# Performance work log

Measured on AMD Instinct MI355X. Metric: run time of the kernel, lower is better.

## Reference

```python
import jax, jax.numpy as jnp
import numpy as np

N_NODES = 200000
N_EDGES = 500000
D = 128          # n_feature = lig_dim = prot_dim
HID = 512        # n_mdn_hidden
N_LAYERS = 3     # n_mdn_layers
G = 10           # n_mdn_gauss
BN_EPS = 1e-5


def setup_inputs() -> dict:
    key = jax.random.key(0)
    ks = jax.random.split(key, 20)
    inp = {
        "h": jax.random.normal(ks[0], (N_NODES, D), dtype=jnp.float32),
        "pl_edge": jax.random.randint(ks[1], (2, N_EDGES), 0, N_NODES),
        "pl_dist": jax.random.uniform(ks[2], (N_EDGES,), dtype=jnp.float32) * 10.0,
        # MLP params
        "W0": jax.random.normal(ks[3], (2 * D, HID), dtype=jnp.float32) * 0.05,
        "b0": jnp.zeros((HID,), dtype=jnp.float32),
        "Wh": jax.random.normal(ks[4], (N_LAYERS - 1, HID, HID), dtype=jnp.float32) * 0.05,
        "bh": jnp.zeros((N_LAYERS - 1, HID), dtype=jnp.float32),
        # BatchNorm1d (eval mode: running stats)
        "bn_gamma": jnp.ones((N_LAYERS, HID), dtype=jnp.float32),
        "bn_beta": jnp.zeros((N_LAYERS, HID), dtype=jnp.float32),
        "bn_mean": jax.random.normal(ks[5], (N_LAYERS, HID), dtype=jnp.float32) * 0.1,
        "bn_var": jax.random.uniform(ks[6], (N_LAYERS, HID), dtype=jnp.float32) + 0.5,
        # GMM heads
        "W_pi": jax.random.normal(ks[7], (HID, G), dtype=jnp.float32) * 0.05,
        "b_pi": jnp.zeros((G,), dtype=jnp.float32),
        "W_sigma": jax.random.normal(ks[8], (HID, G), dtype=jnp.float32) * 0.05,
        "b_sigma": jnp.zeros((G,), dtype=jnp.float32),
        "W_mu": jax.random.normal(ks[9], (HID, G), dtype=jnp.float32) * 0.05,
        "b_mu": jnp.zeros((G,), dtype=jnp.float32),
    }
    return inp


def _bn_eval(x, gamma, beta, mean, var):
    return gamma * (x - mean) * jax.lax.rsqrt(var + BN_EPS) + beta


def reference(h, pl_edge, pl_dist, W0, b0, Wh, bh, bn_gamma, bn_beta,
              bn_mean, bn_var, W_pi, b_pi, W_sigma, b_sigma, W_mu, b_mu):
    # Edge-index gather: ligand feats from edge row 1, protein feats from row 0
    h_l_x = h[pl_edge[1, :]]            # [E, D]
    h_p_x = h[pl_edge[0, :]]            # [E, D]
    C = jnp.concatenate([h_l_x, h_p_x], axis=-1)  # [E, 2D]

    # MLP: (Linear -> BN -> ELU -> Dropout[eval=identity]) x N_LAYERS
    x = C @ W0 + b0
    x = jax.nn.elu(_bn_eval(x, bn_gamma[0], bn_beta[0], bn_mean[0], bn_var[0]))
    for i in range(N_LAYERS - 1):
        x = x @ Wh[i] + bh[i]
        x = jax.nn.elu(_bn_eval(x, bn_gamma[i + 1], bn_beta[i + 1],
                                bn_mean[i + 1], bn_var[i + 1]))

    # GMM heads
    pi = jax.nn.softmax(x @ W_pi + b_pi, axis=-1)          # [E, G]
    sigma = jax.nn.elu(x @ W_sigma + b_sigma) + 1.1        # [E, G]
    mu = jax.nn.elu(x @ W_mu + b_mu) + 1.0                 # [E, G]
    dist = pl_dist[:, None]                                 # [E, 1] (detached)
    return (pi, sigma, mu, dist)
```

## Files before the change

kernel.cpp:

```cpp
#include <hip/hip_runtime.h>
#include <math.h>

typedef __bf16 bf16;
typedef __bf16 bf16x8 __attribute__((ext_vector_type(8)));
typedef float  f32x4  __attribute__((ext_vector_type(4)));

#define E_N    500000
#define NODE_D 128
#define HIDN   512
#define MT     64
#define NTHR   512
#define GRID_MAIN ((E_N + MT - 1) / MT)
#define LOG2E  1.4426950408889634f
#define LN2    0.6931471805599453f

#define WS_WT0   0
#define WS_WT1   262144
#define WS_WT2   786432
#define WS_WTH   1310720
#define WS_BNC   1349632
#define WS_BHEAD 1355776

__device__ __forceinline__ float ldf(const void* p, long i, int bf) {
  if (bf) return (float)((const bf16*)p)[i];
  return ((const float*)p)[i];
}
__device__ __forceinline__ void stf(void* p, long i, float v, int bf) {
  if (bf) ((bf16*)p)[i] = (bf16)v;
  else    ((float*)p)[i] = v;
}
__device__ __forceinline__ int sniff(const void* gma) {
  return (((const unsigned int*)gma)[0] == 0x3F800000u) ? 0 : 1;
}

__global__ void prep_kernel(
    const void* __restrict__ W0, const void* __restrict__ b0,
    const void* __restrict__ Wh, const void* __restrict__ bh,
    const void* __restrict__ gma, const void* __restrict__ bta,
    const void* __restrict__ mean, const void* __restrict__ var,
    const void* __restrict__ Wpi, const void* __restrict__ bpi,
    const void* __restrict__ Wsg, const void* __restrict__ bsg,
    const void* __restrict__ Wmu, const void* __restrict__ bmu,
    bf16* __restrict__ Wt0, bf16* __restrict__ Wt1, bf16* __restrict__ Wt2,
    bf16* __restrict__ WtH, float* __restrict__ bnC, float* __restrict__ bHead)
{
  const int bf = sniff(gma);
  const int idx = blockIdx.x * blockDim.x + threadIdx.x;
  const int T0 = 131072, T1 = T0 + 262144, T2 = T1 + 262144;
  const int T3 = T2 + 16384, T4 = T3 + 1536, T5 = T4 + 32;
  if (idx < T0) {
    int frag = idx >> 9, within = idx & 511;
    int lane = within >> 3, j = within & 7;
    int n = (frag >> 3) * 16 + (lane & 15);
    int k = (frag & 7) * 32 + (lane >> 4) * 8 + j;
    float a = ldf(gma, n, bf) * rsqrtf(ldf(var, n, bf) + 1e-5f);
    Wt0[idx] = (bf16)(ldf(W0, (long)k * 512 + n, bf) * a * LOG2E);
  } else if (idx < T1) {
    int i2 = idx - T0;
    int frag = i2 >> 9, within = i2 & 511;
    int lane = within >> 3, j = within & 7;
    int n = (frag >> 4) * 16 + (lane & 15);
    int k = (frag & 15) * 32 + (lane >> 4) * 8 + j;
    float a = ldf(gma, 512 + n, bf) * rsqrtf(ldf(var, 512 + n, bf) + 1e-5f);
    Wt1[i2] = (bf16)(ldf(Wh, (long)k * 512 + n, bf) * a * LOG2E);
  } else if (idx < T2) {
    int i2 = idx - T1;
    int frag = i2 >> 9, within = i2 & 511;
    int lane = within >> 3, j = within & 7;
    int n = (frag >> 4) * 16 + (lane & 15);
    int k = (frag & 15) * 32 + (lane >> 4) * 8 + j;
    float a = ldf(gma, 1024 + n, bf) * rsqrtf(ldf(var, 1024 + n, bf) + 1e-5f);
    Wt2[i2] = (bf16)(ldf(Wh, 262144L + (long)k * 512 + n, bf) * a * LOG2E);
  } else if (idx < T3) {
    int i2 = idx - T2;
    int frag = i2 >> 9, within = i2 & 511;
    int lane = within >> 3, j = within & 7;
    int c = (frag >> 4) * 16 + (lane & 15);
    int k = (frag & 15) * 32 + (lane >> 4) * 8 + j;
    float v = 0.f;
    if (c < 10)      v = ldf(Wpi, (long)k * 10 + c, bf);
    else if (c < 20) v = ldf(Wsg, (long)k * 10 + (c - 10), bf);
    else if (c < 30) v = ldf(Wmu, (long)k * 10 + (c - 20), bf);
    WtH[i2] = (bf16)v;
  } else if (idx < T4) {
    int j = idx - T3; int l = j >> 9, n = j & 511;
    float g  = ldf(gma, j, bf), be = ldf(bta, j, bf);
    float mn = ldf(mean, j, bf), vr = ldf(var, j, bf);
    float bias = (l == 0) ? ldf(b0, n, bf) : ldf(bh, (long)(l - 1) * 512 + n, bf);
    float a = g * rsqrtf(vr + 1e-5f);
    bnC[j] = (a * (bias - mn) + be) * LOG2E;
  } else if (idx < T5) {
    int c = idx - T4;
    float v = 0.f;
    if (c < 10)      v = ldf(bpi, c, bf);
    else if (c < 20) v = ldf(bsg, c - 10, bf);
    else if (c < 30) v = ldf(bmu, c - 20, bf);
    bHead[c] = v;
  }
}

#define LDA(dst, ks_) do {                                                   \
    _Pragma("unroll")                                                        \
    for (int _nt = 0; _nt < 4; ++_nt)                                        \
      dst[_nt] = *(const bf16x8*)(wptr + (((_nt) * nks + (ks_)) << 9));      \
  } while (0)

#define LDB(dst, ks_) do {                                                   \
    const int _ch = ((((ks_) << 2) + quad) ^ xr) << 4;                       \
    _Pragma("unroll")                                                        \
    for (int _mt = 0; _mt < 4; ++_mt)                                        \
      dst[_mt] = *(const bf16x8*)(xrow + _mt * 16384 + _ch);                 \
  } while (0)

#define MFMA4x4(Ar, Bv) do {                                                 \
    _Pragma("unroll")                                                        \
    for (int _mt = 0; _mt < 4; ++_mt)                                        \
      _Pragma("unroll")                                                      \
      for (int _nt = 0; _nt < 4; ++_nt)                                      \
        acc[_nt][_mt] = __builtin_amdgcn_mfma_f32_16x16x32_bf16(             \
            Ar[_nt], Bv[_mt], acc[_nt][_mt], 0, 0, 0);                       \
  } while (0)

__global__ __launch_bounds__(NTHR, 4) void fused_mdn(
    const void* __restrict__ h, const int* __restrict__ edges,
    const void* __restrict__ dist,
    const bf16* __restrict__ Wt0, const bf16* __restrict__ Wt1,
    const bf16* __restrict__ Wt2, const bf16* __restrict__ WtH,
    const float* __restrict__ bnC, const float* __restrict__ bHead,
    void* __restrict__ out, const void* __restrict__ gma)
{
  __shared__ __align__(16) char smem[64 * 1024];

  const int bf   = sniff(gma);
  const int t    = threadIdx.x;
  const int lane = t & 63;
  const int w    = t >> 6;
  const int l15  = t & 15;
  const int quad = lane >> 4;
  const int xr   = l15 & 7;
  char* const xrow = smem + l15 * 1024;
  const long e0  = (long)blockIdx.x * MT;

  #pragma unroll
  for (int i = 0; i < 4; ++i) {
    int c  = t + i * NTHR;
    int m  = c >> 5;
    int kc = c & 31;
    long e = e0 + m;
    union { uint4 u; bf16x8 v; } val;
    val.u = make_uint4(0u, 0u, 0u, 0u);
    if (e < E_N) {
      int half = kc >> 4;
      int node = edges[(half ? 0L : (long)E_N) + e];
      long off = (long)node * NODE_D + (long)(kc & 15) * 8;
      if (bf) {
        val.u = *(const uint4*)((const bf16*)h + off);
      } else {
        const float4 a = *(const float4*)((const float*)h + off);
        const float4 b = *(const float4*)((const float*)h + off + 4);
        val.v[0] = (bf16)a.x; val.v[1] = (bf16)a.y;
        val.v[2] = (bf16)a.z; val.v[3] = (bf16)a.w;
        val.v[4] = (bf16)b.x; val.v[5] = (bf16)b.y;
        val.v[6] = (bf16)b.z; val.v[7] = (bf16)b.w;
      }
    }
    *(uint4*)(smem + m * 1024 + ((kc ^ (m & 7)) * 16)) = val.u;
  }
  __syncthreads();

  f32x4 acc[4][4];
  const bf16* const Wts[3] = {Wt0, Wt1, Wt2};

  #pragma unroll 1
  for (int layer = 0; layer < 3; ++layer) {
    const int nks = (layer == 0) ? 8 : 16;
    const bf16* const wptr = Wts[layer] + (((w * 4) * nks) << 9) + (lane << 3);

    bf16x8 A0[4], A1[4], B[4];
    LDA(A0, 0);

    f32x4 cvv[4];
    #pragma unroll
    for (int nt = 0; nt < 4; ++nt)
      cvv[nt] = *(const f32x4*)(bnC + layer * HIDN + w * 64 + nt * 16 + quad * 4);

    #pragma unroll
    for (int a = 0; a < 4; ++a)
      #pragma unroll
      for (int b = 0; b < 4; ++b)
        acc[a][b] = cvv[a];

    int ks = 0;
    #pragma unroll 1
    for (; ks < nks - 2; ks += 2) {
      LDB(B, ks);
      LDA(A1, ks + 1);
      MFMA4x4(A0, B);
      LDB(B, ks + 1);
      LDA(A0, ks + 2);
      MFMA4x4(A1, B);
    }
    LDB(B, ks);
    LDA(A1, ks + 1);
    MFMA4x4(A0, B);
    LDB(B, ks + 1);
    MFMA4x4(A1, B);

    __syncthreads();

    #pragma unroll
    for (int nt = 0; nt < 4; ++nt) {
      const int nb = w * 64 + nt * 16 + quad * 4;
      #pragma unroll
      for (int mt = 0; mt < 4; ++mt) {
        const int m = mt * 16 + l15;
        union { bf16 e[4]; uint2 u; } pk;
        #pragma unroll
        for (int j = 0; j < 4; ++j) {
          float tt = acc[nt][mt][j];
          float y = fmaf(fmaxf(tt, 0.f), LN2,
                         __builtin_amdgcn_exp2f(fminf(tt, 0.f))) - 1.f;
          pk.e[j] = (bf16)y;
        }
        int kchunk = (nb >> 3) ^ (m & 7);
        *(uint2*)(smem + m * 1024 + kchunk * 16 + (nb & 7) * 2) = pk.u;
      }
    }
    __syncthreads();
  }

  {
    const int nt = w & 1;
    const int mt = w >> 1;
    const int m  = mt * 16 + l15;
    char* const hrow = xrow + mt * 16384;
    const int cb = nt * 16 + quad * 4;
    f32x4 ha = *(const f32x4*)(bHead + cb);
    const bf16* const hptr = WtH + ((nt * 16) << 9) + (lane << 3);
    bf16x8 hA0, hA1, hB;
    hA0 = *(const bf16x8*)(hptr);
    int ks = 0;
    #pragma unroll 1
    for (; ks < 14; ks += 2) {
      hA1 = *(const bf16x8*)(hptr + ((ks + 1) << 9));
      hB = *(const bf16x8*)(hrow + ((((ks << 2) + quad) ^ xr) << 4));
      ha = __builtin_amdgcn_mfma_f32_16x16x32_bf16(hA0, hB, ha, 0, 0, 0);
      hB = *(const bf16x8*)(hrow + (((((ks + 1) << 2) + quad) ^ xr) << 4));
      hA0 = *(const bf16x8*)(hptr + ((ks + 2) << 9));
      ha = __builtin_amdgcn_mfma_f32_16x16x32_bf16(hA1, hB, ha, 0, 0, 0);
    }
    hA1 = *(const bf16x8*)(hptr + ((ks + 1) << 9));
    hB = *(const bf16x8*)(hrow + ((((ks << 2) + quad) ^ xr) << 4));
    ha = __builtin_amdgcn_mfma_f32_16x16x32_bf16(hA0, hB, ha, 0, 0, 0);
    hB = *(const bf16x8*)(hrow + (((((ks + 1) << 2) + quad) ^ xr) << 4));
    ha = __builtin_amdgcn_mfma_f32_16x16x32_bf16(hA1, hB, ha, 0, 0, 0);

    __syncthreads();

    float* hl = (float*)smem;
    *(f32x4*)(hl + m * 36 + cb) = ha;
  }
  __syncthreads();

  if (t < MT) {
    const long e = e0 + t;
    if (e < E_N) {
      const float* hl = (const float*)smem + t * 36;
      float mx = hl[0];
      #pragma unroll
      for (int g = 1; g < 10; ++g) mx = fmaxf(mx, hl[g]);
      float ex[10], s = 0.f;
      #pragma unroll
      for (int g = 0; g < 10; ++g) { ex[g] = __expf(hl[g] - mx); s += ex[g]; }
      float inv = 1.f / s;
      #pragma unroll
      for (int g = 0; g < 10; ++g) stf(out, e * 10 + g, ex[g] * inv, bf);
      #pragma unroll
      for (int g = 0; g < 10; ++g) {
        float z = hl[10 + g];
        float v = fmaxf(z, 0.f) + __expf(fminf(z, 0.f)) + 0.1f;
        stf(out, 5000000L + e * 10 + g, v, bf);
      }
      #pragma unroll
      for (int g = 0; g < 10; ++g) {
        float z = hl[20 + g];
        float v = fmaxf(z, 0.f) + __expf(fminf(z, 0.f));
        stf(out, 10000000L + e * 10 + g, v, bf);
      }
      stf(out, 15000000L + e, ldf(dist, e, bf), bf);
    }
  }
}

extern "C" void kernel_launch(void* const* d_in, const int* in_sizes, int n_in,
                              void* d_out, int out_size, void* d_ws, size_t ws_size,
                              hipStream_t stream) {
  const void* h    = d_in[0];
  const int*  edg  = (const int*)d_in[1];
  const void* dist = d_in[2];
  const void* W0   = d_in[3];
  const void* b0   = d_in[4];
  const void* Wh   = d_in[5];
  const void* bh   = d_in[6];
  const void* gma  = d_in[7];
  const void* bta  = d_in[8];
  const void* mean = d_in[9];
  const void* var  = d_in[10];
  const void* Wpi  = d_in[11];
  const void* bpi  = d_in[12];
  const void* Wsg  = d_in[13];
  const void* bsg  = d_in[14];
  const void* Wmu  = d_in[15];
  const void* bmu  = d_in[16];

  char* ws = (char*)d_ws;
  bf16*  Wt0 = (bf16*)(ws + WS_WT0);
  bf16*  Wt1 = (bf16*)(ws + WS_WT1);
  bf16*  Wt2 = (bf16*)(ws + WS_WT2);
  bf16*  WtH = (bf16*)(ws + WS_WTH);
  float* bnC = (float*)(ws + WS_BNC);
  float* bHd = (float*)(ws + WS_BHEAD);

  prep_kernel<<<2631, 256, 0, stream>>>(W0, b0, Wh, bh, gma, bta, mean, var,
                                        Wpi, bpi, Wsg, bsg, Wmu, bmu,
                                        Wt0, Wt1, Wt2, WtH, bnC, bHd);

  fused_mdn<<<GRID_MAIN, NTHR, 0, stream>>>(h, edg, dist, Wt0, Wt1, Wt2, WtH,
                                            bnC, bHd, d_out, gma);
}
```

Baseline: 852.6 us.

## Double edge tile per block to 128 to halve weight-fragment reloads

Each block now processes 128 edges instead of 64. Every weight fragment loaded from global memory feeds twice as many MFMAs, and the accumulator array grows to 4x8 tiles. Shared memory moves to 128KB of dynamic LDS, and the launch bound drops to 2 blocks per CU. The head stage is reworked so each wave computes two m-tiles. The aim is to cut repeated L2/global weight traffic across blocks, at the cost of lower occupancy, higher register pressure and half as many blocks.

```diff
diff --git a/kernel.cpp b/kernel.cpp
--- a/kernel.cpp
+++ b/kernel.cpp
@@ -8,7 +8,7 @@
 #define E_N    500000
 #define NODE_D 128
 #define HIDN   512
-#define MT     64
+#define MT     128
 #define NTHR   512
 #define GRID_MAIN ((E_N + MT - 1) / MT)
 #define LOG2E  1.4426950408889634f
@@ -105,23 +105,23 @@
       dst[_nt] = *(const bf16x8*)(wptr + (((_nt) * nks + (ks_)) << 9));      \
   } while (0)
 
-#define LDB(dst, ks_) do {                                                   \
+#define LDB(dst, ks_, half_) do {                                            \
     const int _ch = ((((ks_) << 2) + quad) ^ xr) << 4;                       \
     _Pragma("unroll")                                                        \
     for (int _mt = 0; _mt < 4; ++_mt)                                        \
-      dst[_mt] = *(const bf16x8*)(xrow + _mt * 16384 + _ch);                 \
+      dst[_mt] = *(const bf16x8*)(xrow + ((half_) * 4 + _mt) * 16384 + _ch); \
   } while (0)
 
-#define MFMA4x4(Ar, Bv) do {                                                 \
+#define MFMA4x4(Ar, Bv, half_) do {                                          \
     _Pragma("unroll")                                                        \
     for (int _mt = 0; _mt < 4; ++_mt)                                        \
       _Pragma("unroll")                                                      \
       for (int _nt = 0; _nt < 4; ++_nt)                                      \
-        acc[_nt][_mt] = __builtin_amdgcn_mfma_f32_16x16x32_bf16(             \
-            Ar[_nt], Bv[_mt], acc[_nt][_mt], 0, 0, 0);                       \
+        acc[_nt][(half_) * 4 + _mt] = __builtin_amdgcn_mfma_f32_16x16x32_bf16( \
+            Ar[_nt], Bv[_mt], acc[_nt][(half_) * 4 + _mt], 0, 0, 0);         \
   } while (0)
 
-__global__ __launch_bounds__(NTHR, 4) void fused_mdn(
+__global__ __launch_bounds__(NTHR, 2) void fused_mdn(
     const void* __restrict__ h, const int* __restrict__ edges,
     const void* __restrict__ dist,
     const bf16* __restrict__ Wt0, const bf16* __restrict__ Wt1,
@@ -129,7 +129,7 @@
     const float* __restrict__ bnC, const float* __restrict__ bHead,
     void* __restrict__ out, const void* __restrict__ gma)
 {
-  __shared__ __align__(16) char smem[64 * 1024];
+  extern __shared__ __align__(16) char smem[];
 
   const int bf   = sniff(gma);
   const int t    = threadIdx.x;
@@ -142,7 +142,7 @@
   const long e0  = (long)blockIdx.x * MT;
 
   #pragma unroll
-  for (int i = 0; i < 4; ++i) {
+  for (int i = 0; i < 8; ++i) {
     int c  = t + i * NTHR;
     int m  = c >> 5;
     int kc = c & 31;
@@ -168,7 +168,7 @@
   }
   __syncthreads();
 
-  f32x4 acc[4][4];
+  f32x4 acc[4][8];
   const bf16* const Wts[3] = {Wt0, Wt1, Wt2};
 
   #pragma unroll 1
@@ -187,24 +187,32 @@
     #pragma unroll
     for (int a = 0; a < 4; ++a)
       #pragma unroll
-      for (int b = 0; b < 4; ++b)
+      for (int b = 0; b < 8; ++b)
         acc[a][b] = cvv[a];
 
     int ks = 0;
     #pragma unroll 1
     for (; ks < nks - 2; ks += 2) {
-      LDB(B, ks);
+      LDB(B, ks, 0);
       LDA(A1, ks + 1);
-      MFMA4x4(A0, B);
-      LDB(B, ks + 1);
+      MFMA4x4(A0, B, 0);
+      LDB(B, ks, 1);
+      MFMA4x4(A0, B, 1);
+      LDB(B, ks + 1, 0);
       LDA(A0, ks + 2);
-      MFMA4x4(A1, B);
-    }
-    LDB(B, ks);
+      MFMA4x4(A1, B, 0);
+      LDB(B, ks + 1, 1);
+      MFMA4x4(A1, B, 1);
+    }
+    LDB(B, ks, 0);
     LDA(A1, ks + 1);
-    MFMA4x4(A0, B);
-    LDB(B, ks + 1);
-    MFMA4x4(A1, B);
+    MFMA4x4(A0, B, 0);
+    LDB(B, ks, 1);
+    MFMA4x4(A0, B, 1);
+    LDB(B, ks + 1, 0);
+    MFMA4x4(A1, B, 0);
+    LDB(B, ks + 1, 1);
+    MFMA4x4(A1, B, 1);
 
     __syncthreads();
 
@@ -212,7 +220,7 @@
     for (int nt = 0; nt < 4; ++nt) {
       const int nb = w * 64 + nt * 16 + quad * 4;
       #pragma unroll
-      for (int mt = 0; mt < 4; ++mt) {
+      for (int mt = 0; mt < 8; ++mt) {
         const int m = mt * 16 + l15;
         union { bf16 e[4]; uint2 u; } pk;
         #pragma unroll
@@ -230,35 +238,29 @@
   }
 
   {
-    const int nt = w & 1;
-    const int mt = w >> 1;
-    const int m  = mt * 16 + l15;
-    char* const hrow = xrow + mt * 16384;
-    const int cb = nt * 16 + quad * 4;
-    f32x4 ha = *(const f32x4*)(bHead + cb);
+    const int nt  = w & 1;
+    const int mtp = (w >> 1) * 2;
+    const int m0  = mtp * 16 + l15;
+    const int cb  = nt * 16 + quad * 4;
+    f32x4 ha0 = *(const f32x4*)(bHead + cb);
+    f32x4 ha1 = ha0;
     const bf16* const hptr = WtH + ((nt * 16) << 9) + (lane << 3);
-    bf16x8 hA0, hA1, hB;
-    hA0 = *(const bf16x8*)(hptr);
-    int ks = 0;
-    #pragma unroll 1
-    for (; ks < 14; ks += 2) {
-      hA1 = *(const bf16x8*)(hptr + ((ks + 1) << 9));
-      hB = *(const bf16x8*)(hrow + ((((ks << 2) + quad) ^ xr) << 4));
-      ha = __builtin_amdgcn_mfma_f32_16x16x32_bf16(hA0, hB, ha, 0, 0, 0);
-      hB = *(const bf16x8*)(hrow + (((((ks + 1) << 2) + quad) ^ xr) << 4));
-      hA0 = *(const bf16x8*)(hptr + ((ks + 2) << 9));
-      ha = __builtin_amdgcn_mfma_f32_16x16x32_bf16(hA1, hB, ha, 0, 0, 0);
-    }
-    hA1 = *(const bf16x8*)(hptr + ((ks + 1) << 9));
-    hB = *(const bf16x8*)(hrow + ((((ks << 2) + quad) ^ xr) << 4));
-    ha = __builtin_amdgcn_mfma_f32_16x16x32_bf16(hA0, hB, ha, 0, 0, 0);
-    hB = *(const bf16x8*)(hrow + (((((ks + 1) << 2) + quad) ^ xr) << 4));
-    ha = __builtin_amdgcn_mfma_f32_16x16x32_bf16(hA1, hB, ha, 0, 0, 0);
-
+    char* const hrow0 = xrow + mtp * 16384;
+    char* const hrow1 = xrow + (mtp + 1) * 16384;
+    #pragma unroll 4
+    for (int ks = 0; ks < 16; ++ks) {
+      bf16x8 hA = *(const bf16x8*)(hptr + (ks << 9));
+      const int ch = (((ks << 2) + quad) ^ xr) << 4;
+      bf16x8 hB0 = *(const bf16x8*)(hrow0 + ch);
+      bf16x8 hB1 = *(const bf16x8*)(hrow1 + ch);
+      ha0 = __builtin_amdgcn_mfma_f32_16x16x32_bf16(hA, hB0, ha0, 0, 0, 0);
+      ha1 = __builtin_amdgcn_mfma_f32_16x16x32_bf16(hA, hB1, ha1, 0, 0, 0);
+    }
     __syncthreads();
 
     float* hl = (float*)smem;
-    *(f32x4*)(hl + m * 36 + cb) = ha;
+    *(f32x4*)(hl + m0 * 36 + cb) = ha0;
+    *(f32x4*)(hl + (m0 + 16) * 36 + cb) = ha1;
   }
   __syncthreads();
 
@@ -325,6 +327,7 @@
                                         Wpi, bpi, Wsg, bsg, Wmu, bmu,
                                         Wt0, Wt1, Wt2, WtH, bnC, bHd);
 
-  fused_mdn<<<GRID_MAIN, NTHR, 0, stream>>>(h, edg, dist, Wt0, Wt1, Wt2, WtH,
-                                            bnC, bHd, d_out, gma);
-}
+  fused_mdn<<<GRID_MAIN, NTHR, 128 * 1024, stream>>>(h, edg, dist,
+                                                     Wt0, Wt1, Wt2, WtH,
+                                                     bnC, bHd, d_out, gma);
+}
```

New measurement: 980.2 us. 15.0% more time.

## Switch hidden-layer MFMA from 16x16x32 to 32x32x16 bf16 tiles

Applied to the files above, without the earlier changes.

Replaces the 4x4 grid of 16x16x32 MFMA tiles per wave with a 2x2 grid of 32x32x16 tiles, and re-packs the weight fragments in the prep kernel to match the new operand layout. LDS operand reads and the swizzled epilogue write-back are rewritten for the 32-row lane mapping. The larger instruction needs fewer operand loads per FLOP and fewer MFMA issues, at the cost of a different accumulator layout and possibly different LDS bank-conflict behaviour.

```diff
diff --git a/kernel.cpp b/kernel.cpp
--- a/kernel.cpp
+++ b/kernel.cpp
@@ -4,6 +4,7 @@
 typedef __bf16 bf16;
 typedef __bf16 bf16x8 __attribute__((ext_vector_type(8)));
 typedef float  f32x4  __attribute__((ext_vector_type(4)));
+typedef float  f32x16 __attribute__((ext_vector_type(16)));
 
 #define E_N    500000
 #define NODE_D 128
@@ -51,24 +52,24 @@
   if (idx < T0) {
     int frag = idx >> 9, within = idx & 511;
     int lane = within >> 3, j = within & 7;
-    int n = (frag >> 3) * 16 + (lane & 15);
-    int k = (frag & 7) * 32 + (lane >> 4) * 8 + j;
+    int n = (frag >> 4) * 32 + (lane & 31);
+    int k = (frag & 15) * 16 + (lane >> 5) * 8 + j;
     float a = ldf(gma, n, bf) * rsqrtf(ldf(var, n, bf) + 1e-5f);
     Wt0[idx] = (bf16)(ldf(W0, (long)k * 512 + n, bf) * a * LOG2E);
   } else if (idx < T1) {
     int i2 = idx - T0;
     int frag = i2 >> 9, within = i2 & 511;
     int lane = within >> 3, j = within & 7;
-    int n = (frag >> 4) * 16 + (lane & 15);
-    int k = (frag & 15) * 32 + (lane >> 4) * 8 + j;
+    int n = (frag >> 5) * 32 + (lane & 31);
+    int k = (frag & 31) * 16 + (lane >> 5) * 8 + j;
     float a = ldf(gma, 512 + n, bf) * rsqrtf(ldf(var, 512 + n, bf) + 1e-5f);
     Wt1[i2] = (bf16)(ldf(Wh, (long)k * 512 + n, bf) * a * LOG2E);
   } else if (idx < T2) {
     int i2 = idx - T1;
     int frag = i2 >> 9, within = i2 & 511;
     int lane = within >> 3, j = within & 7;
-    int n = (frag >> 4) * 16 + (lane & 15);
-    int k = (frag & 15) * 32 + (lane >> 4) * 8 + j;
+    int n = (frag >> 5) * 32 + (lane & 31);
+    int k = (frag & 31) * 16 + (lane >> 5) * 8 + j;
     float a = ldf(gma, 1024 + n, bf) * rsqrtf(ldf(var, 1024 + n, bf) + 1e-5f);
     Wt2[i2] = (bf16)(ldf(Wh, 262144L + (long)k * 512 + n, bf) * a * LOG2E);
   } else if (idx < T3) {
@@ -99,26 +100,31 @@
   }
 }
 
-#define LDA(dst, ks_) do {                                                   \
-    _Pragma("unroll")                                                        \
-    for (int _nt = 0; _nt < 4; ++_nt)                                        \
-      dst[_nt] = *(const bf16x8*)(wptr + (((_nt) * nks + (ks_)) << 9));      \
+#define LDA2(dst, u_) do {                                                    \
+    _Pragma("unroll")                                                         \
+    for (int _q = 0; _q < 4; ++_q)                                            \
+      dst[_q] = *(const bf16x8*)(wptr +                                       \
+                 ((((_q >> 1) * nks + (u_) * 2 + (_q & 1))) << 9));           \
   } while (0)
 
-#define LDB(dst, ks_) do {                                                   \
-    const int _ch = ((((ks_) << 2) + quad) ^ xr) << 4;                       \
-    _Pragma("unroll")                                                        \
-    for (int _mt = 0; _mt < 4; ++_mt)                                        \
-      dst[_mt] = *(const bf16x8*)(xrow + _mt * 16384 + _ch);                 \
+#define LDB2(dst, u_) do {                                                    \
+    _Pragma("unroll")                                                         \
+    for (int _p = 0; _p < 4; ++_p) {                                          \
+      const int _ks = (u_) * 2 + (_p & 1);                                    \
+      const int _ch = ((_ks * 2 + hb) ^ xr5) << 4;                            \
+      dst[_p] = *(const bf16x8*)(xrowB + (_p >> 1) * 32768 + _ch);            \
+    }                                                                         \
   } while (0)
 
-#define MFMA4x4(Ar, Bv) do {                                                 \
-    _Pragma("unroll")                                                        \
-    for (int _mt = 0; _mt < 4; ++_mt)                                        \
-      _Pragma("unroll")                                                      \
-      for (int _nt = 0; _nt < 4; ++_nt)                                      \
-        acc[_nt][_mt] = __builtin_amdgcn_mfma_f32_16x16x32_bf16(             \
-            Ar[_nt], Bv[_mt], acc[_nt][_mt], 0, 0, 0);                       \
+#define MFMA8(Ar, Bv) do {                                                    \
+    _Pragma("unroll")                                                         \
+    for (int _kk = 0; _kk < 2; ++_kk)                                         \
+      _Pragma("unroll")                                                       \
+      for (int _mt = 0; _mt < 2; ++_mt)                                       \
+        _Pragma("unroll")                                                     \
+        for (int _nt = 0; _nt < 2; ++_nt)                                     \
+          acc[_nt][_mt] = __builtin_amdgcn_mfma_f32_32x32x16_bf16(            \
+              Ar[_nt * 2 + _kk], Bv[_mt * 2 + _kk], acc[_nt][_mt], 0, 0, 0);  \
   } while (0)
 
 __global__ __launch_bounds__(NTHR, 4) void fused_mdn(
@@ -138,7 +144,11 @@
   const int l15  = t & 15;
   const int quad = lane >> 4;
   const int xr   = l15 & 7;
-  char* const xrow = smem + l15 * 1024;
+  const int l31  = lane & 31;
+  const int hb   = lane >> 5;
+  const int xr5  = lane & 7;
+  char* const xrow  = smem + l15 * 1024;
+  char* const xrowB = smem + l31 * 1024;
   const long e0  = (long)blockIdx.x * MT;
 
   #pragma unroll
@@ -168,62 +178,72 @@
   }
   __syncthreads();
 
-  f32x4 acc[4][4];
+  f32x16 acc[2][2];
   const bf16* const Wts[3] = {Wt0, Wt1, Wt2};
 
   #pragma unroll 1
   for (int layer = 0; layer < 3; ++layer) {
-    const int nks = (layer == 0) ? 8 : 16;
-    const bf16* const wptr = Wts[layer] + (((w * 4) * nks) << 9) + (lane << 3);
+    const int nks = (layer == 0) ? 16 : 32;
+    const int nu  = nks >> 1;
+    const bf16* const wptr = Wts[layer] + (((w * 2) * nks) << 9) + (lane << 3);
 
     bf16x8 A0[4], A1[4], B[4];
-    LDA(A0, 0);
-
-    f32x4 cvv[4];
+    LDA2(A0, 0);
+
+    f32x4 cvv[2][4];
     #pragma unroll
-    for (int nt = 0; nt < 4; ++nt)
-      cvv[nt] = *(const f32x4*)(bnC + layer * HIDN + w * 64 + nt * 16 + quad * 4);
+    for (int nt2 = 0; nt2 < 2; ++nt2)
+      #pragma unroll
+      for (int g = 0; g < 4; ++g)
+        cvv[nt2][g] = *(const f32x4*)(bnC + layer * HIDN +
+                                      w * 64 + nt2 * 32 + g * 8 + hb * 4);
 
     #pragma unroll
-    for (int a = 0; a < 4; ++a)
-      #pragma unroll
-      for (int b = 0; b < 4; ++b)
-        acc[a][b] = cvv[a];
-
-    int ks = 0;
+    for (int nt2 = 0; nt2 < 2; ++nt2)
+      #pragma unroll
+      for (int mt2 = 0; mt2 < 2; ++mt2)
+        #pragma unroll
+        for (int g = 0; g < 4; ++g)
+          #pragma unroll
+          for (int i = 0; i < 4; ++i)
+            acc[nt2][mt2][g * 4 + i] = cvv[nt2][g][i];
+
+    int u = 0;
     #pragma unroll 1
-    for (; ks < nks - 2; ks += 2) {
-      LDB(B, ks);
-      LDA(A1, ks + 1);
-      MFMA4x4(A0, B);
-      LDB(B, ks + 1);
-      LDA(A0, ks + 2);
-      MFMA4x4(A1, B);
-    }
-    LDB(B, ks);
-    LDA(A1, ks + 1);
-    MFMA4x4(A0, B);
-    LDB(B, ks + 1);
-    MFMA4x4(A1, B);
+    for (; u < nu - 2; u += 2) {
+      LDB2(B, u);
+      LDA2(A1, u + 1);
+      MFMA8(A0, B);
+      LDB2(B, u + 1);
+      LDA2(A0, u + 2);
+      MFMA8(A1, B);
+    }
+    LDB2(B, u);
+    LDA2(A1, u + 1);
+    MFMA8(A0, B);
+    LDB2(B, u + 1);
+    MFMA8(A1, B);
 
     __syncthreads();
 
     #pragma unroll
-    for (int nt = 0; nt < 4; ++nt) {
-      const int nb = w * 64 + nt * 16 + quad * 4;
-      #pragma unroll
-      for (int mt = 0; mt < 4; ++mt) {
-        const int m = mt * 16 + l15;
-        union { bf16 e[4]; uint2 u; } pk;
+    for (int nt2 = 0; nt2 < 2; ++nt2) {
+      #pragma unroll
+      for (int mt2 = 0; mt2 < 2; ++mt2) {
+        const int m = mt2 * 32 + l31;
         #pragma unroll
-        for (int j = 0; j < 4; ++j) {
-          float tt = acc[nt][mt][j];
-          float y = fmaf(fmaxf(tt, 0.f), LN2,
-                         __builtin_amdgcn_exp2f(fminf(tt, 0.f))) - 1.f;
-          pk.e[j] = (bf16)y;
+        for (int g = 0; g < 4; ++g) {
+          union { bf16 e[4]; uint2 u; } pk;
+          #pragma unroll
+          for (int j = 0; j < 4; ++j) {
+            float tt = acc[nt2][mt2][g * 4 + j];
+            float y = fmaf(fmaxf(tt, 0.f), LN2,
+                           __builtin_amdgcn_exp2f(fminf(tt, 0.f))) - 1.f;
+            pk.e[j] = (bf16)y;
+          }
+          const int kchunk = (w * 8 + nt2 * 4 + g) ^ (m & 7);
+          *(uint2*)(smem + m * 1024 + kchunk * 16 + hb * 8) = pk.u;
         }
-        int kchunk = (nb >> 3) ^ (m & 7);
-        *(uint2*)(smem + m * 1024 + kchunk * 16 + (nb & 7) * 2) = pk.u;
       }
     }
     __syncthreads();
```

New measurement: 931.8 us. 1.09x slower.

## Overlap ELU epilogue of previous layer with next layer's MFMA K-loop via banded columns

Applied to the files above, without the earlier changes.

Each wave now owns 16-column slices in four 128-wide bands instead of a contiguous 64-column block. With two accumulator sets, the ELU/bf16 write-back of band b from the previous layer can be interleaved into the MFMA segment of the next layer that only reads K-chunks from already-finished bands. The K-loops are fully unrolled into 4-step segments separated by barriers, and the head GEMM is overlapped with the last layer's epilogue the same way. The aim is to hide epilogue ALU and LDS-write latency behind matrix work. In exchange it doubles accumulator registers (risking spills or lower occupancy under the 4-block launch bound) and adds more barriers.

```diff
diff --git a/kernel.cpp b/kernel.cpp
--- a/kernel.cpp
+++ b/kernel.cpp
@@ -102,7 +102,7 @@
 #define LDA(dst, ks_) do {                                                   \
     _Pragma("unroll")                                                        \
     for (int _nt = 0; _nt < 4; ++_nt)                                        \
-      dst[_nt] = *(const bf16x8*)(wptr + (((_nt) * nks + (ks_)) << 9));      \
+      dst[_nt] = *(const bf16x8*)(wp + ((_nt * wstr + (ks_)) << 9));         \
   } while (0)
 
 #define LDB(dst, ks_) do {                                                   \
@@ -112,13 +112,78 @@
       dst[_mt] = *(const bf16x8*)(xrow + _mt * 16384 + _ch);                 \
   } while (0)
 
-#define MFMA4x4(Ar, Bv) do {                                                 \
+#define MFMA16(ACC, Ar, Bv) do {                                             \
     _Pragma("unroll")                                                        \
     for (int _mt = 0; _mt < 4; ++_mt)                                        \
       _Pragma("unroll")                                                      \
       for (int _nt = 0; _nt < 4; ++_nt)                                      \
-        acc[_nt][_mt] = __builtin_amdgcn_mfma_f32_16x16x32_bf16(             \
-            Ar[_nt], Bv[_mt], acc[_nt][_mt], 0, 0, 0);                       \
+        ACC[_nt][_mt] = __builtin_amdgcn_mfma_f32_16x16x32_bf16(             \
+            Ar[_nt], Bv[_mt], ACC[_nt][_mt], 0, 0, 0);                       \
+  } while (0)
+
+#define EPI_UNIT(P, nt_, mt_) do {                                           \
+    const int _nb = (nt_) * 128 + w * 16 + quad * 4;                         \
+    const int _m  = (mt_) * 16 + l15;                                        \
+    union { bf16 e[4]; uint2 u; } _pk;                                       \
+    _Pragma("unroll")                                                        \
+    for (int _j = 0; _j < 4; ++_j) {                                         \
+      float _t = P[nt_][mt_][_j];                                            \
+      float _y = fmaf(fmaxf(_t, 0.f), LN2,                                   \
+                      __builtin_amdgcn_exp2f(fminf(_t, 0.f))) - 1.f;         \
+      _pk.e[_j] = (bf16)_y;                                                  \
+    }                                                                        \
+    const int _kc = (_nb >> 3) ^ (_m & 7);                                   \
+    *(uint2*)(smem + _m * 1024 + _kc * 16 + (_nb & 7) * 2) = _pk.u;          \
+  } while (0)
+
+#define EPI_BAND(P, b_) do {                                                 \
+    EPI_UNIT(P, b_, 0); EPI_UNIT(P, b_, 1);                                  \
+    EPI_UNIT(P, b_, 2); EPI_UNIT(P, b_, 3);                                  \
+  } while (0)
+
+#define GSEG4(ACCc, ACCp, band_, s0_, DO_EPI, DO_PRIME) do {                 \
+    LDB(B, (s0_));     LDA(A1, (s0_) + 1);                                   \
+    if (DO_EPI) EPI_UNIT(ACCp, band_, 0);                                    \
+    MFMA16(ACCc, A0, B);                                                     \
+    LDB(B, (s0_) + 1); LDA(A0, (s0_) + 2);                                   \
+    if (DO_EPI) EPI_UNIT(ACCp, band_, 1);                                    \
+    MFMA16(ACCc, A1, B);                                                     \
+    LDB(B, (s0_) + 2); LDA(A1, (s0_) + 3);                                   \
+    if (DO_EPI) EPI_UNIT(ACCp, band_, 2);                                    \
+    MFMA16(ACCc, A0, B);                                                     \
+    LDB(B, (s0_) + 3);                                                       \
+    if (DO_PRIME) LDA(A0, (s0_) + 4);                                        \
+    if (DO_EPI) EPI_UNIT(ACCp, band_, 3);                                    \
+    MFMA16(ACCc, A1, B);                                                     \
+  } while (0)
+
+#define HSEG4(band_, s0_, DO_EPI, DO_PRIME) do {                             \
+    hB = *(const bf16x8*)(hrow + (((((s0_) << 2) + quad) ^ xr) << 4));       \
+    hA1 = *(const bf16x8*)(hptr + (((s0_) + 1) << 9));                       \
+    if (DO_EPI) EPI_UNIT(accA, band_, 0);                                    \
+    ha = __builtin_amdgcn_mfma_f32_16x16x32_bf16(hA0, hB, ha, 0, 0, 0);      \
+    hB = *(const bf16x8*)(hrow + ((((((s0_) + 1) << 2) + quad) ^ xr) << 4)); \
+    hA0 = *(const bf16x8*)(hptr + (((s0_) + 2) << 9));                       \
+    if (DO_EPI) EPI_UNIT(accA, band_, 1);                                    \
+    ha = __builtin_amdgcn_mfma_f32_16x16x32_bf16(hA1, hB, ha, 0, 0, 0);      \
+    hB = *(const bf16x8*)(hrow + ((((((s0_) + 2) << 2) + quad) ^ xr) << 4)); \
+    hA1 = *(const bf16x8*)(hptr + (((s0_) + 3) << 9));                       \
+    if (DO_EPI) EPI_UNIT(accA, band_, 2);                                    \
+    ha = __builtin_amdgcn_mfma_f32_16x16x32_bf16(hA0, hB, ha, 0, 0, 0);      \
+    hB = *(const bf16x8*)(hrow + ((((((s0_) + 3) << 2) + quad) ^ xr) << 4)); \
+    if (DO_PRIME) hA0 = *(const bf16x8*)(hptr + (((s0_) + 4) << 9));         \
+    if (DO_EPI) EPI_UNIT(accA, band_, 3);                                    \
+    ha = __builtin_amdgcn_mfma_f32_16x16x32_bf16(hA1, hB, ha, 0, 0, 0);      \
+  } while (0)
+
+#define ACC_INIT(ACC, layer_) do {                                           \
+    _Pragma("unroll")                                                        \
+    for (int _nt = 0; _nt < 4; ++_nt) {                                      \
+      const f32x4 _cv = *(const f32x4*)(bnC + (layer_) * HIDN +              \
+                                        _nt * 128 + w * 16 + quad * 4);      \
+      _Pragma("unroll")                                                      \
+      for (int _mt = 0; _mt < 4; ++_mt) ACC[_nt][_mt] = _cv;                 \
+    }                                                                        \
   } while (0)
 
 __global__ __launch_bounds__(NTHR, 4) void fused_mdn(
@@ -166,68 +231,53 @@
     }
     *(uint4*)(smem + m * 1024 + ((kc ^ (m & 7)) * 16)) = val.u;
   }
-  __syncthreads();
-
-  f32x4 acc[4][4];
-  const bf16* const Wts[3] = {Wt0, Wt1, Wt2};
-
-  #pragma unroll 1
-  for (int layer = 0; layer < 3; ++layer) {
-    const int nks = (layer == 0) ? 8 : 16;
-    const bf16* const wptr = Wts[layer] + (((w * 4) * nks) << 9) + (lane << 3);
-
-    bf16x8 A0[4], A1[4], B[4];
-    LDA(A0, 0);
-
-    f32x4 cvv[4];
-    #pragma unroll
-    for (int nt = 0; nt < 4; ++nt)
-      cvv[nt] = *(const f32x4*)(bnC + layer * HIDN + w * 64 + nt * 16 + quad * 4);
-
-    #pragma unroll
-    for (int a = 0; a < 4; ++a)
-      #pragma unroll
-      for (int b = 0; b < 4; ++b)
-        acc[a][b] = cvv[a];
-
-    int ks = 0;
-    #pragma unroll 1
-    for (; ks < nks - 2; ks += 2) {
-      LDB(B, ks);
-      LDA(A1, ks + 1);
-      MFMA4x4(A0, B);
-      LDB(B, ks + 1);
-      LDA(A0, ks + 2);
-      MFMA4x4(A1, B);
-    }
-    LDB(B, ks);
-    LDA(A1, ks + 1);
-    MFMA4x4(A0, B);
-    LDB(B, ks + 1);
-    MFMA4x4(A1, B);
-
-    __syncthreads();
-
-    #pragma unroll
-    for (int nt = 0; nt < 4; ++nt) {
-      const int nb = w * 64 + nt * 16 + quad * 4;
-      #pragma unroll
-      for (int mt = 0; mt < 4; ++mt) {
-        const int m = mt * 16 + l15;
-        union { bf16 e[4]; uint2 u; } pk;
-        #pragma unroll
-        for (int j = 0; j < 4; ++j) {
-          float tt = acc[nt][mt][j];
-          float y = fmaf(fmaxf(tt, 0.f), LN2,
-                         __builtin_amdgcn_exp2f(fminf(tt, 0.f))) - 1.f;
-          pk.e[j] = (bf16)y;
-        }
-        int kchunk = (nb >> 3) ^ (m & 7);
-        *(uint2*)(smem + m * 1024 + kchunk * 16 + (nb & 7) * 2) = pk.u;
-      }
-    }
-    __syncthreads();
-  }
+
+  f32x4 accA[4][4], accB[4][4];
+  bf16x8 A0[4], A1[4], B[4];
+  const bf16* wp;
+  int wstr;
+
+  wp = Wt0 + ((w * 8) << 9) + (lane << 3);
+  wstr = 64;
+  __syncthreads();
+  LDA(A0, 0);
+  ACC_INIT(accA, 0);
+  GSEG4(accA, accA, 0, 0, false, true);
+  GSEG4(accA, accA, 0, 4, false, false);
+  __syncthreads();
+
+  EPI_BAND(accA, 0);
+  wp = Wt1 + ((w * 16) << 9) + (lane << 3);
+  wstr = 128;
+  LDA(A0, 0);
+  ACC_INIT(accB, 1);
+  __syncthreads();
+
+  GSEG4(accB, accA, 1, 0,  true,  true);
+  __syncthreads();
+  GSEG4(accB, accA, 2, 4,  true,  true);
+  __syncthreads();
+  GSEG4(accB, accA, 3, 8,  true,  true);
+  __syncthreads();
+  GSEG4(accB, accA, 0, 12, false, false);
+
+  EPI_BAND(accB, 0);
+  wp = Wt2 + ((w * 16) << 9) + (lane << 3);
+  wstr = 128;
+  LDA(A0, 0);
+  ACC_INIT(accA, 2);
+  __syncthreads();
+
+  GSEG4(accA, accB, 1, 0,  true,  true);
+  __syncthreads();
+  GSEG4(accA, accB, 2, 4,  true,  true);
+  __syncthreads();
+  GSEG4(accA, accB, 3, 8,  true,  true);
+  __syncthreads();
+  GSEG4(accA, accB, 0, 12, false, false);
+
+  EPI_BAND(accA, 0);
+  __syncthreads();
 
   {
     const int nt = w & 1;
@@ -239,22 +289,13 @@
     const bf16* const hptr = WtH + ((nt * 16) << 9) + (lane << 3);
     bf16x8 hA0, hA1, hB;
     hA0 = *(const bf16x8*)(hptr);
-    int ks = 0;
-    #pragma unroll 1
-    for (; ks < 14; ks += 2) {
-      hA1 = *(const bf16x8*)(hptr + ((ks + 1) << 9));
-      hB = *(const bf16x8*)(hrow + ((((ks << 2) + quad) ^ xr) << 4));
-      ha = __builtin_amdgcn_mfma_f32_16x16x32_bf16(hA0, hB, ha, 0, 0, 0);
-      hB = *(const bf16x8*)(hrow + (((((ks + 1) << 2) + quad) ^ xr) << 4));
-      hA0 = *(const bf16x8*)(hptr + ((ks + 2) << 9));
-      ha = __builtin_amdgcn_mfma_f32_16x16x32_bf16(hA1, hB, ha, 0, 0, 0);
-    }
-    hA1 = *(const bf16x8*)(hptr + ((ks + 1) << 9));
-    hB = *(const bf16x8*)(hrow + ((((ks << 2) + quad) ^ xr) << 4));
-    ha = __builtin_amdgcn_mfma_f32_16x16x32_bf16(hA0, hB, ha, 0, 0, 0);
-    hB = *(const bf16x8*)(hrow + (((((ks + 1) << 2) + quad) ^ xr) << 4));
-    ha = __builtin_amdgcn_mfma_f32_16x16x32_bf16(hA1, hB, ha, 0, 0, 0);
-
+    HSEG4(1, 0, true, true);
+    __syncthreads();
+    HSEG4(2, 4, true, true);
+    __syncthreads();
+    HSEG4(3, 8, true, true);
+    __syncthreads();
+    HSEG4(0, 12, false, false);
     __syncthreads();
 
     float* hl = (float*)smem;
```

Result: slower. 1.186 ms (+39.1%).
